# Kernel optimization log

Measured on AMD Instinct MI355X. Metric: run time of the kernel, lower is better.

## Reference

```python
import jax, jax.numpy as jnp
import numpy as np
from jax import lax

WIN = 11  # window_size


def _uniform_filter_valid(x, win):
    """Separable uniform (box) filter, VALID padding. x: [B,1,H,W].
    Equivalent to scipy uniform_filter followed by skimage's pad-cropping,
    since cropped positions only use fully-interior windows."""
    kh = jnp.full((1, 1, win, 1), 1.0 / win, dtype=x.dtype)
    kw = jnp.full((1, 1, 1, win), 1.0 / win, dtype=x.dtype)
    dn = ('NCHW', 'OIHW', 'NCHW')
    x = lax.conv_general_dilated(x, kh, (1, 1), 'VALID', dimension_numbers=dn)
    x = lax.conv_general_dilated(x, kw, (1, 1), 'VALID', dimension_numbers=dn)
    return x


def _ssim_loss(pred, target, win):
    # skimage structural_similarity with gaussian_weights=False, data_range=1.0
    data_range = 1.0
    C1 = (0.01 * data_range) ** 2
    C2 = (0.03 * data_range) ** 2
    NP = win * win
    cov_norm = NP / (NP - 1.0)  # sample covariance correction

    uf = lambda z: _uniform_filter_valid(z, win)
    ux = uf(pred)
    uy = uf(target)
    uxx = uf(pred * pred)
    uyy = uf(target * target)
    uxy = uf(pred * target)

    vx = cov_norm * (uxx - ux * ux)
    vy = cov_norm * (uyy - uy * uy)
    vxy = cov_norm * (uxy - ux * uy)

    A1 = 2.0 * ux * uy + C1
    A2 = 2.0 * vxy + C2
    B1 = ux * ux + uy * uy + C1
    B2 = vx + vy + C2
    S = (A1 * A2) / (B1 * B2)

    # mean SSIM per image, then mean over batch (identical to flat mean here)
    return 1.0 - jnp.mean(S)


def setup_inputs() -> dict:
    key = jax.random.key(0)
    k1, k2 = jax.random.split(key)
    B, C, H, W = 32, 1, 512, 512
    pred = jax.random.uniform(k1, (B, C, H, W), dtype=jnp.float32)
    target = jax.random.uniform(k2, (B, C, H, W), dtype=jnp.float32)
    return {"pred": pred, "target": target}


def reference(pred, target):
    return _ssim_loss(pred, target, WIN)
```

## Files before the change

### kernel.cpp

```cpp
#include <hip/hip_runtime.h>


#define WW 512
#define OH 502
#define BANDR 44
#define INV_N (1.0f / 8064128.0f)

#define DPP_ADD(x, ctrl, rmask)                                            \
    x += __int_as_float(__builtin_amdgcn_update_dpp(                       \
        0, __float_as_int(x), (ctrl), (rmask), 0xf, true))

__device__ __forceinline__ float wave_iscan(float x) {
    DPP_ADD(x, 0x111, 0xf);
    DPP_ADD(x, 0x112, 0xf);
    DPP_ADD(x, 0x114, 0xf);
    DPP_ADD(x, 0x118, 0xf);
    DPP_ADD(x, 0x142, 0xa);
    DPP_ADD(x, 0x143, 0xc);
    return x;
}

__device__ __forceinline__ float2 hwin(float v0, float v1, int lane) {
    float e = v0 + v1;
    float S = wave_iscan(e);
    float A4 = __shfl(S, lane + 4);
    float A5 = __shfl(S, lane + 5);
    float v5 = __shfl(v0, lane + 5);
    float W0 = A4 - S + e + v5;
    float W1 = A5 - S + v1;
    return make_float2(W0, W1);
}

__device__ __forceinline__ float ssim_term(float s0, float s1, float sq, float sx) {
    const float NP  = 121.f;
    const float cn  = 121.f / 120.f;
    const float C1n = 1e-4f * 121.f * 121.f;
    const float C2n = 9e-4f * 121.f * 121.f;
    float m1 = s0 * s1;
    float q1 = fmaf(s0, s0, s1 * s1);
    float A1 = fmaf(2.f, m1, C1n);
    float B1 = q1 + C1n;
    float A2 = fmaf(2.f * cn, fmaf(NP, sx, -m1), C2n);
    float B2 = fmaf(cn, fmaf(NP, sq, -q1), C2n);
    return A1 * A2 * __builtin_amdgcn_rcpf(B1 * B2);
}

__global__ __launch_bounds__(256)
void ssim_main(const float* __restrict__ Pg, const float* __restrict__ Tg,
               float* __restrict__ outp) {
    const int tid  = threadIdx.x;
    const int lane = tid & 63;
    const int wv   = tid >> 6;
    const int Wid  = blockIdx.x * 4 + wv;
    const int img   = Wid / 60;
    const int rem   = Wid - img * 60;
    const int strip = rem / 12;
    const int band  = rem - strip * 12;

    const int col0 = (strip == 4) ? 472 : strip * 118;
    const int outw = (strip == 4) ? 30 : 118;
    const int y0   = band * BANDR;
    const int rows = min(BANDR, OH - y0);

    const int cload = min(col0 + 2 * lane, 510);
    const bool ok   = lane < (outw >> 1);

    const float* Pb = Pg + img * (WW * WW);
    const float* Tb = Tg + img * (WW * WW);

    float2 prr[11], trr[11];
    float sp0 = 0.f, sp1 = 0.f, st0 = 0.f, st1 = 0.f;
    float sq0 = 0.f, sq1 = 0.f, sx0 = 0.f, sx1 = 0.f;

    #pragma unroll
    for (int r = 0; r < 10; ++r) {
        float2 p = *(const float2*)(Pb + (y0 + r) * WW + cload);
        float2 t = *(const float2*)(Tb + (y0 + r) * WW + cload);
        prr[r] = p; trr[r] = t;
        sp0 += p.x; sp1 += p.y; st0 += t.x; st1 += t.y;
        sq0 = fmaf(p.x, p.x, sq0); sq0 = fmaf(t.x, t.x, sq0);
        sq1 = fmaf(p.y, p.y, sq1); sq1 = fmaf(t.y, t.y, sq1);
        sx0 = fmaf(p.x, t.x, sx0); sx1 = fmaf(p.y, t.y, sx1);
    }
    float2 Pn = *(const float2*)(Pb + (y0 + 10) * WW + cload);
    float2 Tn = *(const float2*)(Tb + (y0 + 10) * WW + cload);

    float acc = 0.f;

    for (int yy = 0; yy < rows; yy += 11) {
        #pragma unroll
        for (int j = 0; j < 11; ++j) {
            if (yy + j < rows) {
                const int sn = (10 + j) % 11;
                prr[sn] = Pn; trr[sn] = Tn;
                sp0 += Pn.x; sp1 += Pn.y; st0 += Tn.x; st1 += Tn.y;
                sq0 = fmaf(Pn.x, Pn.x, sq0); sq0 = fmaf(Tn.x, Tn.x, sq0);
                sq1 = fmaf(Pn.y, Pn.y, sq1); sq1 = fmaf(Tn.y, Tn.y, sq1);
                sx0 = fmaf(Pn.x, Tn.x, sx0); sx1 = fmaf(Pn.y, Tn.y, sx1);
                int nr = min(y0 + 11 + yy + j, 511);
                Pn = *(const float2*)(Pb + nr * WW + cload);
                Tn = *(const float2*)(Tb + nr * WW + cload);
                float2 w0 = hwin(sp0, sp1, lane);
                float2 w1 = hwin(st0, st1, lane);
                float2 w2 = hwin(sq0, sq1, lane);
                float2 w3 = hwin(sx0, sx1, lane);
                if (ok) {
                    acc += ssim_term(w0.x, w1.x, w2.x, w3.x);
                    acc += ssim_term(w0.y, w1.y, w2.y, w3.y);
                }
                float2 po = prr[j], to = trr[j];
                sp0 -= po.x; sp1 -= po.y; st0 -= to.x; st1 -= to.y;
                sq0 = fmaf(po.x, -po.x, sq0); sq0 = fmaf(to.x, -to.x, sq0);
                sq1 = fmaf(po.y, -po.y, sq1); sq1 = fmaf(to.y, -to.y, sq1);
                sx0 = fmaf(po.x, -to.x, sx0); sx1 = fmaf(po.y, -to.y, sx1);
            }
        }
    }

    #pragma unroll
    for (int off = 32; off > 0; off >>= 1) acc += __shfl_down(acc, off);
    __shared__ float wred[4];
    if (lane == 0) wred[wv] = acc;
    __syncthreads();
    if (tid == 0) {
        float s = wred[0] + wred[1] + wred[2] + wred[3];
        float contrib = -s * INV_N;
        if (blockIdx.x == 0) contrib += 1.0f;
        atomicAdd(outp, contrib);
    }
}

extern "C" void kernel_launch(void* const* d_in, const int* in_sizes, int n_in,
                              void* d_out, int out_size, void* d_ws, size_t ws_size,
                              hipStream_t stream) {
    const float* pred = (const float*)d_in[0];
    const float* targ = (const float*)d_in[1];
    float* out = (float*)d_out;

    hipMemsetAsync(out, 0, sizeof(float), stream);
    ssim_main<<<dim3(480), dim3(256), 0, stream>>>(pred, targ, out);
}
```

Before: 108.2 us.

## Process two output rows per iteration with deeper row prefetch

```diff
diff --git a/kernel.cpp b/kernel.cpp
--- a/kernel.cpp
+++ b/kernel.cpp
@@ -4,6 +4,7 @@
 #define WW 512
 #define OH 502
 #define BANDR 44
+#define NBANDS 12
 #define INV_N (1.0f / 8064128.0f)
 
 #define DPP_ADD(x, ctrl, rmask)                                            \
@@ -45,7 +46,7 @@
     return A1 * A2 * __builtin_amdgcn_rcpf(B1 * B2);
 }
 
-__global__ __launch_bounds__(256)
+__global__ __launch_bounds__(256, 1)
 void ssim_main(const float* __restrict__ Pg, const float* __restrict__ Tg,
                float* __restrict__ outp) {
     const int tid  = threadIdx.x;
@@ -54,8 +55,8 @@
     const int Wid  = blockIdx.x * 4 + wv;
     const int img   = Wid / 60;
     const int rem   = Wid - img * 60;
-    const int strip = rem / 12;
-    const int band  = rem - strip * 12;
+    const int strip = rem / NBANDS;
+    const int band  = rem - strip * NBANDS;
 
     const int col0 = (strip == 4) ? 472 : strip * 118;
     const int outw = (strip == 4) ? 30 : 118;
@@ -82,37 +83,74 @@
         sq1 = fmaf(p.y, p.y, sq1); sq1 = fmaf(t.y, t.y, sq1);
         sx0 = fmaf(p.x, t.x, sx0); sx1 = fmaf(p.y, t.y, sx1);
     }
-    float2 Pn = *(const float2*)(Pb + (y0 + 10) * WW + cload);
-    float2 Tn = *(const float2*)(Tb + (y0 + 10) * WW + cload);
+    float2 PA0 = *(const float2*)(Pb + (y0 + 10) * WW + cload);
+    float2 TA0 = *(const float2*)(Tb + (y0 + 10) * WW + cload);
+    float2 PB0 = *(const float2*)(Pb + (y0 + 11) * WW + cload);
+    float2 TB0 = *(const float2*)(Tb + (y0 + 11) * WW + cload);
+    float2 PA1 = *(const float2*)(Pb + min(y0 + 12, 511) * WW + cload);
+    float2 TA1 = *(const float2*)(Tb + min(y0 + 12, 511) * WW + cload);
+    float2 PB1 = *(const float2*)(Pb + min(y0 + 13, 511) * WW + cload);
+    float2 TB1 = *(const float2*)(Tb + min(y0 + 13, 511) * WW + cload);
 
     float acc = 0.f;
 
-    for (int yy = 0; yy < rows; yy += 11) {
+    for (int blk = 0; blk < 2; ++blk) {
         #pragma unroll
-        for (int j = 0; j < 11; ++j) {
-            if (yy + j < rows) {
-                const int sn = (10 + j) % 11;
-                prr[sn] = Pn; trr[sn] = Tn;
-                sp0 += Pn.x; sp1 += Pn.y; st0 += Tn.x; st1 += Tn.y;
-                sq0 = fmaf(Pn.x, Pn.x, sq0); sq0 = fmaf(Tn.x, Tn.x, sq0);
-                sq1 = fmaf(Pn.y, Pn.y, sq1); sq1 = fmaf(Tn.y, Tn.y, sq1);
-                sx0 = fmaf(Pn.x, Tn.x, sx0); sx1 = fmaf(Pn.y, Tn.y, sx1);
-                int nr = min(y0 + 11 + yy + j, 511);
-                Pn = *(const float2*)(Pb + nr * WW + cload);
-                Tn = *(const float2*)(Tb + nr * WW + cload);
-                float2 w0 = hwin(sp0, sp1, lane);
-                float2 w1 = hwin(st0, st1, lane);
-                float2 w2 = hwin(sq0, sq1, lane);
-                float2 w3 = hwin(sx0, sx1, lane);
+        for (int p = 0; p < 11; ++p) {
+            if (22 * blk + 2 * p < rows) {
+                const int sa = (10 + 2 * p) % 11;
+                const int sb = (2 * p) % 11;
+                const int sc = (2 * p + 1) % 11;
+                float2 Pa = PA0, Ta = TA0, Pc = PB0, Tc = TB0;
+                PA0 = PA1; TA0 = TA1; PB0 = PB1; TB0 = TB1;
+                int nb = y0 + 14 + 22 * blk + 2 * p;
+                int r1 = min(nb, 511), r2 = min(nb + 1, 511);
+                PA1 = *(const float2*)(Pb + r1 * WW + cload);
+                TA1 = *(const float2*)(Tb + r1 * WW + cload);
+                PB1 = *(const float2*)(Pb + r2 * WW + cload);
+                TB1 = *(const float2*)(Tb + r2 * WW + cload);
+
+                prr[sa] = Pa; trr[sa] = Ta;
+                float a_sp0 = sp0 + Pa.x, a_sp1 = sp1 + Pa.y;
+                float a_st0 = st0 + Ta.x, a_st1 = st1 + Ta.y;
+                float a_sq0 = fmaf(Pa.x, Pa.x, fmaf(Ta.x, Ta.x, sq0));
+                float a_sq1 = fmaf(Pa.y, Pa.y, fmaf(Ta.y, Ta.y, sq1));
+                float a_sx0 = fmaf(Pa.x, Ta.x, sx0);
+                float a_sx1 = fmaf(Pa.y, Ta.y, sx1);
+                float2 wa0 = hwin(a_sp0, a_sp1, lane);
+                float2 wa1 = hwin(a_st0, a_st1, lane);
+                float2 wa2 = hwin(a_sq0, a_sq1, lane);
+                float2 wa3 = hwin(a_sx0, a_sx1, lane);
+
+                float2 po = prr[sb], to = trr[sb];
+                prr[sb] = Pc; trr[sb] = Tc;
+                float b_sp0 = a_sp0 - po.x + Pc.x, b_sp1 = a_sp1 - po.y + Pc.y;
+                float b_st0 = a_st0 - to.x + Tc.x, b_st1 = a_st1 - to.y + Tc.y;
+                float b_sq0 = fmaf(Pc.x, Pc.x, fmaf(Tc.x, Tc.x,
+                              fmaf(po.x, -po.x, fmaf(to.x, -to.x, a_sq0))));
+                float b_sq1 = fmaf(Pc.y, Pc.y, fmaf(Tc.y, Tc.y,
+                              fmaf(po.y, -po.y, fmaf(to.y, -to.y, a_sq1))));
+                float b_sx0 = fmaf(Pc.x, Tc.x, fmaf(po.x, -to.x, a_sx0));
+                float b_sx1 = fmaf(Pc.y, Tc.y, fmaf(po.y, -to.y, a_sx1));
+                float2 wb0 = hwin(b_sp0, b_sp1, lane);
+                float2 wb1 = hwin(b_st0, b_st1, lane);
+                float2 wb2 = hwin(b_sq0, b_sq1, lane);
+                float2 wb3 = hwin(b_sx0, b_sx1, lane);
+
                 if (ok) {
-                    acc += ssim_term(w0.x, w1.x, w2.x, w3.x);
-                    acc += ssim_term(w0.y, w1.y, w2.y, w3.y);
+                    acc += ssim_term(wa0.x, wa1.x, wa2.x, wa3.x);
+                    acc += ssim_term(wa0.y, wa1.y, wa2.y, wa3.y);
+                    acc += ssim_term(wb0.x, wb1.x, wb2.x, wb3.x);
+                    acc += ssim_term(wb0.y, wb1.y, wb2.y, wb3.y);
                 }
-                float2 po = prr[j], to = trr[j];
-                sp0 -= po.x; sp1 -= po.y; st0 -= to.x; st1 -= to.y;
-                sq0 = fmaf(po.x, -po.x, sq0); sq0 = fmaf(to.x, -to.x, sq0);
-                sq1 = fmaf(po.y, -po.y, sq1); sq1 = fmaf(to.y, -to.y, sq1);
-                sx0 = fmaf(po.x, -to.x, sx0); sx1 = fmaf(po.y, -to.y, sx1);
+
+                float2 po2 = prr[sc], to2 = trr[sc];
+                sp0 = b_sp0 - po2.x; sp1 = b_sp1 - po2.y;
+                st0 = b_st0 - to2.x; st1 = b_st1 - to2.y;
+                sq0 = fmaf(po2.x, -po2.x, fmaf(to2.x, -to2.x, b_sq0));
+                sq1 = fmaf(po2.y, -po2.y, fmaf(to2.y, -to2.y, b_sq1));
+                sx0 = fmaf(po2.x, -to2.x, b_sx0);
+                sx1 = fmaf(po2.y, -to2.y, b_sx1);
             }
         }
     }
```

Measured after the change: 110.3 us. Within noise of the previous version (+2.0%).
